# Performance work log

Measured on AMD Instinct MI355X. Metric: run time of the kernel, lower is better.

Reference implementation:

```python
import jax, jax.numpy as jnp
import numpy as np

HIDDEN = 2048
NUM_HEADS = 16
HEAD_DIM = HIDDEN // NUM_HEADS


def setup_inputs() -> dict:
    key = jax.random.key(0)
    ks = jax.random.split(key, 5)
    B, S, H = 2, 2048, HIDDEN
    # xavier_uniform bounds
    qkv_bound = float(np.sqrt(6.0 / (H + 3 * H)))
    out_bound = float(np.sqrt(6.0 / (H + H)))
    return {
        "x": jax.random.normal(ks[0], (B, S, H), dtype=jnp.float32),
        "W_qkv": jax.random.uniform(ks[1], (3 * H, H), minval=-qkv_bound, maxval=qkv_bound, dtype=jnp.float32),
        "b_qkv": jnp.zeros((3 * H,), dtype=jnp.float32),
        "W_out": jax.random.uniform(ks[2], (H, H), minval=-out_bound, maxval=out_bound, dtype=jnp.float32),
        "b_out": jnp.zeros((H,), dtype=jnp.float32),
    }


def reference(x, W_qkv, b_qkv, W_out, b_out):
    B, S, H = x.shape
    # fused QKV projection (torch Linear: x @ W.T + b)
    qkv = x @ W_qkv.T + b_qkv                      # (B, S, 3H)
    q, k, v = jnp.split(qkv, 3, axis=-1)
    # (B, S, H) -> (B, N, S, D)
    def to_heads(t):
        return t.reshape(B, S, NUM_HEADS, HEAD_DIM).transpose(0, 2, 1, 3)
    q, k, v = to_heads(q), to_heads(k), to_heads(v)
    scale = HEAD_DIM ** -0.5
    scores = jnp.einsum("bnqd,bnkd->bnqk", q, k) * scale  # (B, N, S, S)
    causal = jnp.triu(jnp.ones((S, S), dtype=bool), k=1)
    scores = jnp.where(causal, -jnp.inf, scores)
    attn = jax.nn.softmax(scores, axis=-1)
    out = jnp.einsum("bnqk,bnkd->bnqd", attn, v)           # (B, N, S, D)
    out = out.transpose(0, 2, 1, 3).reshape(B, S, H)
    return out @ W_out.T + b_out
```

## Files before the change

### kernel.cpp

```cpp
#include <hip/hip_runtime.h>
#include <stdint.h>


using bf16x8 = __attribute__((ext_vector_type(8))) __bf16;
using f32x4  = __attribute__((ext_vector_type(4))) float;

#define S_LEN 2048
#define HID   2048
#define NHEAD 16
#define DHEAD 128
#define KDIM  2048
#define QSCALE_L2E (0.08838834764831845f * 1.4426950408889634f)

__device__ __forceinline__ unsigned short f2bf(float f) {
  union { float f; unsigned int u; } c; c.f = f;
  unsigned int u = c.u;
  return (unsigned short)((u + 0x7FFFu + ((u >> 16) & 1u)) >> 16);
}

__device__ __forceinline__ unsigned int pkbf(float a, float b) {
  union { __bf16 h[2]; unsigned int u; } x;
  x.h[0] = (__bf16)a; x.h[1] = (__bf16)b;
  return x.u;
}

__device__ __forceinline__ void gload_lds16(const void* g, void* l) {
  __builtin_amdgcn_global_load_lds(
      (const __attribute__((address_space(1))) unsigned int*)g,
      (__attribute__((address_space(3))) unsigned int*)l, 16, 0, 0);
}

__device__ __forceinline__ f32x4 mfma16(bf16x8 a, bf16x8 b, f32x4 c) {
  return __builtin_amdgcn_mfma_f32_16x16x32_bf16(a, b, c, 0, 0, 0);
}

__device__ __forceinline__ float hmax4(f32x4 v) {
  return fmaxf(fmaxf(v[0], v[1]), fmaxf(v[2], v[3]));
}

__global__ void cvt_bf16(const float* __restrict__ in, unsigned short* __restrict__ out, int n) {
  const int n4 = n >> 2;
  const int stride = gridDim.x * blockDim.x;
  for (int i = blockIdx.x * blockDim.x + threadIdx.x; i < n4; i += stride) {
    float4 v = reinterpret_cast<const float4*>(in)[i];
    ushort4 o;
    o.x = f2bf(v.x); o.y = f2bf(v.y); o.z = f2bf(v.z); o.w = f2bf(v.w);
    reinterpret_cast<ushort4*>(out)[i] = o;
  }
}

__global__ __launch_bounds__(512, 2) void gemm_qkv8(
    const unsigned short* __restrict__ A, const unsigned short* __restrict__ Bw,
    const float* __restrict__ bias,
    unsigned short* __restrict__ q_out, unsigned short* __restrict__ k_out,
    unsigned short* __restrict__ vt_out)
{
  __shared__ char lsA[2][32768];
  __shared__ char lsB[2][32768];
  const int tid = threadIdx.x, l = tid & 63, w = tid >> 6;
  const int wr = w >> 2, wc = w & 3;
  const int row16 = l & 15, kg = l >> 4;

  const int bid = blockIdx.x;
  const int swz = (bid & 7) * 48 + (bid >> 3);
  const int bm = (swz & 15) * 256, bn = (swz >> 4) * 256;
  const char* Ag = (const char*)A + (size_t)bm * (KDIM * 2);
  const char* Bg = (const char*)Bw + (size_t)bn * (KDIM * 2);

  f32x4 acc[8][4] = {};

  float bv[4];
  #pragma unroll
  for (int j = 0; j < 4; ++j) bv[j] = bias[bn + wc * 64 + j * 16 + row16];
  asm volatile("" :: "v"(bv[0]), "v"(bv[1]), "v"(bv[2]), "v"(bv[3]));

#define BAR   asm volatile("s_barrier" ::: "memory")
#define LGKM0 asm volatile("s_waitcnt lgkmcnt(0)" ::: "memory"); __builtin_amdgcn_sched_barrier(0)
#define VM4   asm volatile("s_waitcnt vmcnt(4)" ::: "memory")
#define PRIO1 __builtin_amdgcn_s_setprio(1)
#define PRIO0 __builtin_amdgcn_s_setprio(0)

#define STAGE_A(buf, k0, qa) do {                                              \
    _Pragma("unroll")                                                          \
    for (int p = 0; p < 2; ++p) {                                              \
      const int o = tid * 16;                                                  \
      const int r = p * 128 + (qa) * 64 + (o >> 7);                            \
      const int cb = (o & 127) ^ ((r & 7) << 4);                               \
      gload_lds16(Ag + (size_t)r * (KDIM * 2) + (k0) * 2 + cb,                 \
                  lsA[buf] + p * 16384 + (qa) * 8192 + o);                     \
    } } while (0)

#define STAGE_B(buf, k0, qb) do {                                              \
    _Pragma("unroll")                                                          \
    for (int p = 0; p < 2; ++p) {                                              \
      const int o = tid * 16;                                                  \
      const int blk = o >> 12;                                                 \
      const int r = p * 128 + blk * 64 + (qb) * 32 + ((o >> 7) & 31);          \
      const int cb = (o & 127) ^ ((r & 7) << 4);                               \
      gload_lds16(Bg + (size_t)r * (KDIM * 2) + (k0) * 2 + cb,                 \
                  lsB[buf] + p * 16384 + blk * 8192 + (qb) * 4096 + (o & 4095)); \
    } } while (0)

#define RD_A(dst, i0) do { _Pragma("unroll")                                   \
    for (int i = 0; i < 4; ++i) {                                              \
      const int m = wr * 128 + ((i0) + i) * 16 + row16;                        \
      _Pragma("unroll")                                                        \
      for (int h = 0; h < 2; ++h)                                              \
        dst[i][h] = *(const bf16x8*)(Ac + m * 128 + ((h * 64 + kg * 16) ^ ((m & 7) << 4))); \
    } } while (0)

#define RD_B(dst, j0) do { _Pragma("unroll")                                   \
    for (int j = 0; j < 2; ++j) {                                              \
      const int n = wc * 64 + ((j0) + j) * 16 + row16;                         \
      _Pragma("unroll")                                                        \
      for (int h = 0; h < 2; ++h)                                              \
        dst[j][h] = *(const bf16x8*)(Bc + n * 128 + ((h * 64 + kg * 16) ^ ((n & 7) << 4))); \
    } } while (0)

#define MM(afrag, bfrag, i0, j0) do { _Pragma("unroll")                        \
    for (int i = 0; i < 4; ++i) { _Pragma("unroll")                            \
      for (int j = 0; j < 2; ++j) { _Pragma("unroll")                          \
        for (int h = 0; h < 2; ++h)                                            \
          acc[(i0) + i][(j0) + j] = mfma16(afrag[i][h], bfrag[j][h], acc[(i0) + i][(j0) + j]); \
    } } } while (0)

  STAGE_A(0, 0, 0); STAGE_B(0, 0, 0); STAGE_A(0, 0, 1); STAGE_B(0, 0, 1);
  asm volatile("s_waitcnt vmcnt(0)" ::: "memory");
  BAR;

  bf16x8 afl[4][2], afh[4][2], bfl[2][2], bfh[2][2];
  constexpr int NCH = KDIM / 64;

  #pragma unroll 1
  for (int t = 0; t < NCH - 1; ++t) {
    const int cur = t & 1, nxt = cur ^ 1;
    const char* Ac = lsA[cur];
    const char* Bc = lsB[cur];
    const int k1 = (t + 1) * 64;
    RD_A(afl, 0); RD_B(bfl, 0);
    STAGE_A(nxt, k1, 0);
    BAR; LGKM0;
    PRIO1; MM(afl, bfl, 0, 0); PRIO0;
    VM4; BAR;
    RD_A(afh, 4);
    STAGE_B(nxt, k1, 0);
    BAR; LGKM0;
    PRIO1; MM(afh, bfl, 4, 0); PRIO0;
    VM4; BAR;
    RD_B(bfh, 2);
    STAGE_A(nxt, k1, 1);
    BAR; LGKM0;
    PRIO1; MM(afl, bfh, 0, 2); PRIO0;
    BAR;
    STAGE_B(nxt, k1, 1);
    BAR;
    PRIO1; MM(afh, bfh, 4, 2); PRIO0;
    VM4; BAR;
  }
  {
    const char* Ac = lsA[(NCH - 1) & 1];
    const char* Bc = lsB[(NCH - 1) & 1];
    RD_A(afl, 0); RD_B(bfl, 0);
    MM(afl, bfl, 0, 0);
    asm volatile("s_waitcnt vmcnt(2)" ::: "memory");
    RD_A(afh, 4);
    MM(afh, bfl, 4, 0);
    asm volatile("s_waitcnt vmcnt(0)" ::: "memory");
    RD_B(bfh, 2);
    MM(afl, bfh, 0, 2);
    MM(afh, bfh, 4, 2);
  }
#undef STAGE_A
#undef STAGE_B
#undef RD_A
#undef RD_B
#undef MM
#undef BAR
#undef LGKM0
#undef VM4
#undef PRIO1
#undef PRIO0

  #pragma unroll
  for (int i = 0; i < 8; ++i) {
    const int row = bm + wr * 128 + i * 16 + kg * 4;
    #pragma unroll
    for (int j = 0; j < 4; ++j) {
      const int col = bn + wc * 64 + j * 16 + row16;
      const int sec = col >> 11;
      const int within = col & 2047;
      const int head = within >> 7, d = within & 127;
      #pragma unroll
      for (int r = 0; r < 4; ++r) {
        const int rr = row + r;
        const int b = rr >> 11, s = rr & 2047;
        const int bh = b * NHEAD + head;
        const float v = acc[i][j][r] + bv[j];
        if (sec == 0)
          q_out[((size_t)bh * S_LEN + s) * DHEAD + d] = f2bf(v * QSCALE_L2E);
        else if (sec == 1)
          k_out[((size_t)bh * S_LEN + s) * DHEAD + d] = f2bf(v);
        else
          vt_out[((size_t)bh * DHEAD + d) * S_LEN + s] = f2bf(v);
      }
    }
  }
}

__global__ __launch_bounds__(256) void gemm_out(
    const unsigned short* __restrict__ A, const unsigned short* __restrict__ Bw,
    const float* __restrict__ bias, float* __restrict__ c_out)
{
  constexpr int K = KDIM, N = HID;
  __shared__ char lsA[128 * 128];
  __shared__ char lsB[128 * 128];
  const int tid = threadIdx.x;
  const int l = tid & 63, w = tid >> 6;
  const int wr = w >> 1, wc = w & 1;
  const int bm = blockIdx.x * 128, bn = blockIdx.y * 128;
  const int row16 = l & 15, kg = l >> 4;

  f32x4 acc[4][4] = {};

  for (int k0 = 0; k0 < K; k0 += 64) {
    #pragma unroll
    for (int c = 0; c < 4; ++c) {
      const int o = c * 4096 + tid * 16;
      const int r = o >> 7;
      const int cb = (o & 127) ^ ((r & 7) << 4);
      gload_lds16((const char*)A + ((size_t)(bm + r) * K + k0) * 2 + cb,
                  lsA + c * 4096 + (w << 10));
      gload_lds16((const char*)Bw + ((size_t)(bn + r) * K + k0) * 2 + cb,
                  lsB + c * 4096 + (w << 10));
    }
    __syncthreads();

    #pragma unroll
    for (int h = 0; h < 2; ++h) {
      bf16x8 af[4], bfr[4];
      #pragma unroll
      for (int i = 0; i < 4; ++i) {
        const int ra = wr * 64 + i * 16 + row16;
        af[i]  = *(const bf16x8*)(lsA + ra * 128 + ((h * 64 + kg * 16) ^ ((ra & 7) << 4)));
        const int rb = wc * 64 + i * 16 + row16;
        bfr[i] = *(const bf16x8*)(lsB + rb * 128 + ((h * 64 + kg * 16) ^ ((rb & 7) << 4)));
      }
      #pragma unroll
      for (int i = 0; i < 4; ++i)
        #pragma unroll
        for (int j = 0; j < 4; ++j)
          acc[i][j] = mfma16(af[i], bfr[j], acc[i][j]);
    }
    __syncthreads();
  }

  #pragma unroll
  for (int i = 0; i < 4; ++i) {
    const int row = bm + wr * 64 + i * 16 + kg * 4;
    #pragma unroll
    for (int j = 0; j < 4; ++j) {
      const int col = bn + wc * 64 + j * 16 + row16;
      const float bvj = bias[col];
      #pragma unroll
      for (int r = 0; r < 4; ++r)
        c_out[(size_t)(row + r) * N + col] = acc[i][j][r] + bvj;
    }
  }
}

__global__ __launch_bounds__(256, 2) void attn_fwd(
    const unsigned short* __restrict__ Q, const unsigned short* __restrict__ Kk,
    const unsigned short* __restrict__ Vt, unsigned short* __restrict__ O)
{
  __shared__ char lsK[2][64 * 256];
  __shared__ char lsV[2][128 * 128];
  __shared__ char lsP[4][32 * 128];
  const int tid = threadIdx.x, l = tid & 63, w = tid >> 6;
  const int row16 = l & 15, kg = l >> 4;
  const int qb = (blockIdx.y < 16) ? (15 - (int)blockIdx.x) : (int)blockIdx.x;
  const int bh = blockIdx.y;
  const int bidx = bh >> 4, head = bh & 15;

  const char* Qh = (const char*)(Q  + (size_t)bh * S_LEN * DHEAD);
  const char* Kh = (const char*)(Kk + (size_t)bh * S_LEN * DHEAD);
  const char* Vh = (const char*)(Vt + (size_t)bh * DHEAD * S_LEN);

  const int q0w = qb * 128 + w * 32;

  bf16x8 qf[2][4];
  #pragma unroll
  for (int qs = 0; qs < 2; ++qs)
    #pragma unroll
    for (int t = 0; t < 4; ++t)
      qf[qs][t] = *(const bf16x8*)(Qh + ((size_t)(q0w + qs * 16 + row16) * DHEAD + t * 32 + kg * 8) * 2);

  float m[2]  = {-1e30f, -1e30f};
  float ls[2] = {0.f, 0.f};
  f32x4 oacc[2][8] = {};

  const int last = 2 * qb + 1;

#define STAGE(buf, kt_) do {                                                     \
    _Pragma("unroll")                                                            \
    for (int c = 0; c < 4; ++c) {                                                \
      const int o = c * 4096 + tid * 16;                                         \
      const int rk = o >> 8, cbk = (o & 255) ^ ((rk & 7) << 4);                  \
      gload_lds16(Kh + (size_t)((kt_) * 64 + rk) * 256 + cbk,                    \
                  lsK[buf] + c * 4096 + (w << 10));                              \
      const int dv = o >> 7, cbv = (o & 127) ^ ((dv & 7) << 4);                  \
      gload_lds16(Vh + (size_t)dv * 4096 + (size_t)(kt_) * 128 + cbv,            \
                  lsV[buf] + c * 4096 + (w << 10));                              \
    } } while (0)

  STAGE(0, 0);
  __syncthreads();

  int cur = 0;
  for (int kt = 0; ; ++kt) {
    if (kt < last) STAGE(cur ^ 1, kt + 1);

    if (kt * 64 <= q0w + 31) {
      const char* Kc = lsK[cur];
      const char* Vc = lsV[cur];
      char* Pl = lsP[w];

      f32x4 sc[4][2] = {};
      #pragma unroll
      for (int j = 0; j < 4; ++j) {
        const int krow = j * 16 + row16;
        const int sw = (krow & 7) << 4;
        bf16x8 kf[4];
        #pragma unroll
        for (int t = 0; t < 4; ++t)
          kf[t] = *(const bf16x8*)(Kc + krow * 256 + ((t * 64 + kg * 16) ^ sw));
        #pragma unroll
        for (int t = 0; t < 4; ++t) {
          sc[j][0] = mfma16(kf[t], qf[0][t], sc[j][0]);
          sc[j][1] = mfma16(kf[t], qf[1][t], sc[j][1]);
        }
      }

      if (kt >= 2 * qb) {
        #pragma unroll
        for (int j = 0; j < 4; ++j) {
          const int kvb = kt * 64 + j * 16 + kg * 4;
          #pragma unroll
          for (int qs = 0; qs < 2; ++qs) {
            const int qq = q0w + qs * 16 + row16;
            #pragma unroll
            for (int r = 0; r < 4; ++r)
              if (kvb + r > qq) sc[j][qs][r] = -1e30f;
          }
        }
      }

      float pm[2], al[2] = {1.f, 1.f};
      #pragma unroll
      for (int qs = 0; qs < 2; ++qs) {
        float mx = fmaxf(fmaxf(hmax4(sc[0][qs]), hmax4(sc[1][qs])),
                         fmaxf(hmax4(sc[2][qs]), hmax4(sc[3][qs])));
        mx = fmaxf(mx, __shfl_xor(mx, 16, 64));
        mx = fmaxf(mx, __shfl_xor(mx, 32, 64));
        pm[qs] = mx;
      }
      const bool need = (pm[0] > m[0] + 8.f) || (pm[1] > m[1] + 8.f);
      if (__any(need)) {
        const float n0 = fmaxf(m[0], pm[0]), n1 = fmaxf(m[1], pm[1]);
        al[0] = exp2f(m[0] - n0); al[1] = exp2f(m[1] - n1);
        m[0] = n0; m[1] = n1;
        float aq[2][4];
        #pragma unroll
        for (int qs2 = 0; qs2 < 2; ++qs2)
          #pragma unroll
          for (int r = 0; r < 4; ++r)
            aq[qs2][r] = __shfl(al[qs2], kg * 4 + r, 64);
        #pragma unroll
        for (int qs2 = 0; qs2 < 2; ++qs2)
          #pragma unroll
          for (int dt = 0; dt < 8; ++dt)
            #pragma unroll
            for (int r = 0; r < 4; ++r)
              oacc[qs2][dt][r] *= aq[qs2][r];
      }

      #pragma unroll
      for (int qs = 0; qs < 2; ++qs) {
        const int q = qs * 16 + row16;
        const int psw = (q & 7) << 4;
        float ps = 0.f;
        #pragma unroll
        for (int j = 0; j < 4; ++j) {
          const float p0 = exp2f(sc[j][qs][0] - m[qs]);
          const float p1 = exp2f(sc[j][qs][1] - m[qs]);
          const float p2 = exp2f(sc[j][qs][2] - m[qs]);
          const float p3 = exp2f(sc[j][qs][3] - m[qs]);
          ps += (p0 + p1) + (p2 + p3);
          uint2 pw; pw.x = pkbf(p0, p1); pw.y = pkbf(p2, p3);
          *(uint2*)(Pl + q * 128 + ((j * 32 + kg * 8) ^ psw)) = pw;
        }
        ps += __shfl_xor(ps, 16, 64);
        ps += __shfl_xor(ps, 32, 64);
        ls[qs] = ls[qs] * al[qs] + ps;
      }

      bf16x8 pa[2][2];
      #pragma unroll
      for (int qs2 = 0; qs2 < 2; ++qs2) {
        const int q = qs2 * 16 + row16;
        #pragma unroll
        for (int ks = 0; ks < 2; ++ks)
          pa[qs2][ks] = *(const bf16x8*)(Pl + q * 128 + ((ks * 64 + kg * 16) ^ ((q & 7) << 4)));
      }
      #pragma unroll
      for (int dt = 0; dt < 8; ++dt) {
        const int drow = dt * 16 + row16;
        const int vsw = (drow & 7) << 4;
        bf16x8 v0 = *(const bf16x8*)(Vc + drow * 128 + ((kg * 16) ^ vsw));
        bf16x8 v1 = *(const bf16x8*)(Vc + drow * 128 + ((64 + kg * 16) ^ vsw));
        oacc[0][dt] = mfma16(pa[0][0], v0, oacc[0][dt]);
        oacc[0][dt] = mfma16(pa[0][1], v1, oacc[0][dt]);
        oacc[1][dt] = mfma16(pa[1][0], v0, oacc[1][dt]);
        oacc[1][dt] = mfma16(pa[1][1], v1, oacc[1][dt]);
      }
    }

    __syncthreads();
    if (kt == last) break;
    cur ^= 1;
  }
#undef STAGE

  #pragma unroll
  for (int qs2 = 0; qs2 < 2; ++qs2) {
    #pragma unroll
    for (int r = 0; r < 4; ++r) {
      const float lr = __shfl(ls[qs2], kg * 4 + r, 64);
      const float inv = 1.0f / lr;
      const int q = q0w + qs2 * 16 + kg * 4 + r;
      const size_t orow = (size_t)(bidx * S_LEN + q) * HID + (size_t)head * DHEAD;
      #pragma unroll
      for (int dt = 0; dt < 8; ++dt)
        O[orow + dt * 16 + row16] = f2bf(oacc[qs2][dt][r] * inv);
    }
  }
}

extern "C" void kernel_launch(void* const* d_in, const int* in_sizes, int n_in,
                              void* d_out, int out_size, void* d_ws, size_t ws_size,
                              hipStream_t stream) {
  const float* x    = (const float*)d_in[0];
  const float* Wqkv = (const float*)d_in[1];
  const float* bqkv = (const float*)d_in[2];
  const float* Wout = (const float*)d_in[3];
  const float* bout = (const float*)d_in[4];
  float* out = (float*)d_out;

  if (ws_size < 100663296) return;
  char* ws = (char*)d_ws;
  unsigned short* Qb    = (unsigned short*)(ws);
  unsigned short* Kb    = (unsigned short*)(ws + 16777216);
  unsigned short* Vtb   = (unsigned short*)(ws + 2 * 16777216);
  unsigned short* xb    = (unsigned short*)(ws + 3 * 16777216);
  unsigned short* Ob    = xb;
  unsigned short* Wqkvb = (unsigned short*)(ws + 4 * 16777216);
  unsigned short* Woutb = (unsigned short*)(ws + 4 * 16777216 + 25165824);

  cvt_bf16<<<2048, 256, 0, stream>>>(x,    xb,    4096 * 2048);
  cvt_bf16<<<2048, 256, 0, stream>>>(Wqkv, Wqkvb, 6144 * 2048);
  cvt_bf16<<<1024, 256, 0, stream>>>(Wout, Woutb, 2048 * 2048);

  gemm_qkv8<<<384, 512, 0, stream>>>(xb, Wqkvb, bqkv, Qb, Kb, Vtb);
  attn_fwd<<<dim3(16, 32), 256, 0, stream>>>(Qb, Kb, Vtb, Ob);
  gemm_out<<<dim3(32, 16), 256, 0, stream>>>(Ob, Woutb, bout, out);
}
```

Before: 317.4 us.

## Deepen QKV GEMM prefetch pipeline with half-tile LDS staging and unrolled loop

Restructures the QKV projection GEMM's shared-memory staging so each buffer is split into independently loaded halves. Prefetch now runs up to one and a half chunks ahead instead of one, with vmcnt(6) waits. The main loop is unrolled by two so buffer indices are compile-time constants, and the bias load moves into the epilogue. The goal is to hide global-load latency behind MFMA work, at the cost of more complex barrier ordering and more in-flight loads that could race if the waits are miscounted.

Measured after the change: 314.0 us. No clear change (-1.1%).

```diff
diff --git a/kernel.cpp b/kernel.cpp
--- a/kernel.cpp
+++ b/kernel.cpp
@@ -49,7 +49,14 @@
   }
 }
 
-__global__ __launch_bounds__(512, 2) void gemm_qkv8(
+#define BAR   asm volatile("s_barrier" ::: "memory")
+#define LGKM0 do { asm volatile("s_waitcnt lgkmcnt(0)" ::: "memory"); \
+                   __builtin_amdgcn_sched_barrier(0); } while (0)
+#define VM(n) asm volatile("s_waitcnt vmcnt(" #n ")" ::: "memory")
+#define PRIO1 __builtin_amdgcn_s_setprio(1)
+#define PRIO0 __builtin_amdgcn_s_setprio(0)
+
+__global__ __launch_bounds__(512, 2) void gemm_qkv(
     const unsigned short* __restrict__ A, const unsigned short* __restrict__ Bw,
     const float* __restrict__ bias,
     unsigned short* __restrict__ q_out, unsigned short* __restrict__ k_out,
@@ -69,139 +76,166 @@
 
   f32x4 acc[8][4] = {};
 
-  float bv[4];
-  #pragma unroll
-  for (int j = 0; j < 4; ++j) bv[j] = bias[bn + wc * 64 + j * 16 + row16];
-  asm volatile("" :: "v"(bv[0]), "v"(bv[1]), "v"(bv[2]), "v"(bv[3]));
-
-#define BAR   asm volatile("s_barrier" ::: "memory")
-#define LGKM0 asm volatile("s_waitcnt lgkmcnt(0)" ::: "memory"); __builtin_amdgcn_sched_barrier(0)
-#define VM4   asm volatile("s_waitcnt vmcnt(4)" ::: "memory")
-#define PRIO1 __builtin_amdgcn_s_setprio(1)
-#define PRIO0 __builtin_amdgcn_s_setprio(0)
-
-#define STAGE_A(buf, k0, qa) do {                                              \
-    _Pragma("unroll")                                                          \
+#define STAGE_A(cc, h) do { _Pragma("unroll")                                  \
     for (int p = 0; p < 2; ++p) {                                              \
-      const int o = tid * 16;                                                  \
-      const int r = p * 128 + (qa) * 64 + (o >> 7);                            \
-      const int cb = (o & 127) ^ ((r & 7) << 4);                               \
-      gload_lds16(Ag + (size_t)r * (KDIM * 2) + (k0) * 2 + cb,                 \
-                  lsA[buf] + p * 16384 + (qa) * 8192 + o);                     \
+      const int o = p * 8192 + tid * 16;                                       \
+      const int lr = o >> 7;                                                   \
+      const int m = ((lr >> 6) << 7) + (h) * 64 + (lr & 63);                   \
+      const int cb = (o & 127) ^ ((m & 7) << 4);                               \
+      gload_lds16(Ag + (size_t)m * (KDIM * 2) + (size_t)(cc) * 128 + cb,       \
+                  lsA[(cc) & 1] + (h) * 16384 + p * 8192 + (w << 10));         \
     } } while (0)
 
-#define STAGE_B(buf, k0, qb) do {                                              \
-    _Pragma("unroll")                                                          \
+#define STAGE_B(cc, h) do { _Pragma("unroll")                                  \
     for (int p = 0; p < 2; ++p) {                                              \
-      const int o = tid * 16;                                                  \
-      const int blk = o >> 12;                                                 \
-      const int r = p * 128 + blk * 64 + (qb) * 32 + ((o >> 7) & 31);          \
-      const int cb = (o & 127) ^ ((r & 7) << 4);                               \
-      gload_lds16(Bg + (size_t)r * (KDIM * 2) + (k0) * 2 + cb,                 \
-                  lsB[buf] + p * 16384 + blk * 8192 + (qb) * 4096 + (o & 4095)); \
+      const int o = p * 8192 + tid * 16;                                       \
+      const int lr = o >> 7;                                                   \
+      const int n = ((lr >> 5) << 6) + (h) * 32 + (lr & 31);                   \
+      const int cb = (o & 127) ^ ((n & 7) << 4);                               \
+      gload_lds16(Bg + (size_t)n * (KDIM * 2) + (size_t)(cc) * 128 + cb,       \
+                  lsB[(cc) & 1] + (h) * 16384 + p * 8192 + (w << 10));         \
     } } while (0)
 
-#define RD_A(dst, i0) do { _Pragma("unroll")                                   \
+#define RD_A(dst, i0, buf) do { _Pragma("unroll")                              \
     for (int i = 0; i < 4; ++i) {                                              \
       const int m = wr * 128 + ((i0) + i) * 16 + row16;                        \
+      const char* base = lsA[buf] + (((m >> 6) & 1) * 16384)                   \
+                       + (((m >> 7) & 1) * 8192) + ((m & 63) * 128);           \
       _Pragma("unroll")                                                        \
       for (int h = 0; h < 2; ++h)                                              \
-        dst[i][h] = *(const bf16x8*)(Ac + m * 128 + ((h * 64 + kg * 16) ^ ((m & 7) << 4))); \
+        dst[i][h] = *(const bf16x8*)(base +                                    \
+                    ((h * 64 + kg * 16) ^ ((m & 7) << 4)));                    \
     } } while (0)
 
-#define RD_B(dst, j0) do { _Pragma("unroll")                                   \
+#define RD_B(dst, j0, buf) do { _Pragma("unroll")                              \
     for (int j = 0; j < 2; ++j) {                                              \
       const int n = wc * 64 + ((j0) + j) * 16 + row16;                         \
+      const char* base = lsB[buf] + (((n >> 5) & 1) * 16384)                   \
+                       + ((n >> 6) * 4096) + ((n & 31) * 128);                 \
       _Pragma("unroll")                                                        \
       for (int h = 0; h < 2; ++h)                                              \
-        dst[j][h] = *(const bf16x8*)(Bc + n * 128 + ((h * 64 + kg * 16) ^ ((n & 7) << 4))); \
+        dst[j][h] = *(const bf16x8*)(base +                                    \
+                    ((h * 64 + kg * 16) ^ ((n & 7) << 4)));                    \
     } } while (0)
 
-#define MM(afrag, bfrag, i0, j0) do { _Pragma("unroll")                        \
+#define MM(af, bf, i0, j0) do { _Pragma("unroll")                              \
     for (int i = 0; i < 4; ++i) { _Pragma("unroll")                            \
       for (int j = 0; j < 2; ++j) { _Pragma("unroll")                          \
         for (int h = 0; h < 2; ++h)                                            \
-          acc[(i0) + i][(j0) + j] = mfma16(afrag[i][h], bfrag[j][h], acc[(i0) + i][(j0) + j]); \
+          acc[(i0) + i][(j0) + j] =                                            \
+            mfma16(af[i][h], bf[j][h], acc[(i0) + i][(j0) + j]);               \
     } } } while (0)
 
-  STAGE_A(0, 0, 0); STAGE_B(0, 0, 0); STAGE_A(0, 0, 1); STAGE_B(0, 0, 1);
-  asm volatile("s_waitcnt vmcnt(0)" ::: "memory");
+  STAGE_A(0, 0); STAGE_B(0, 0); STAGE_A(0, 1); STAGE_B(0, 1);
+  STAGE_A(1, 0); STAGE_B(1, 0); STAGE_A(1, 1);
+  VM(6);
   BAR;
 
-  bf16x8 afl[4][2], afh[4][2], bfl[2][2], bfh[2][2];
-  constexpr int NCH = KDIM / 64;
+  bf16x8 alo[4][2], ahi[4][2], blo[2][2], bhi[2][2];
 
   #pragma unroll 1
-  for (int t = 0; t < NCH - 1; ++t) {
-    const int cur = t & 1, nxt = cur ^ 1;
-    const char* Ac = lsA[cur];
-    const char* Bc = lsB[cur];
-    const int k1 = (t + 1) * 64;
-    RD_A(afl, 0); RD_B(bfl, 0);
-    STAGE_A(nxt, k1, 0);
-    BAR; LGKM0;
-    PRIO1; MM(afl, bfl, 0, 0); PRIO0;
-    VM4; BAR;
-    RD_A(afh, 4);
-    STAGE_B(nxt, k1, 0);
-    BAR; LGKM0;
-    PRIO1; MM(afh, bfl, 4, 0); PRIO0;
-    VM4; BAR;
-    RD_B(bfh, 2);
-    STAGE_A(nxt, k1, 1);
-    BAR; LGKM0;
-    PRIO1; MM(afl, bfh, 0, 2); PRIO0;
-    BAR;
-    STAGE_B(nxt, k1, 1);
-    BAR;
-    PRIO1; MM(afh, bfh, 4, 2); PRIO0;
-    VM4; BAR;
+  for (int i = 0; i < 15; ++i) {
+    const int t0 = 2 * i;
+    RD_A(alo, 0, 0); RD_B(blo, 0, 0);
+    STAGE_B(t0 + 1, 1);
+    BAR; LGKM0;
+    PRIO1; MM(alo, blo, 0, 0); PRIO0;
+    BAR;
+    RD_A(ahi, 4, 0);
+    STAGE_A(t0 + 2, 0);
+    BAR; LGKM0;
+    PRIO1; MM(ahi, blo, 4, 0); PRIO0;
+    BAR;
+    RD_B(bhi, 2, 0);
+    STAGE_B(t0 + 2, 0);
+    BAR; LGKM0;
+    PRIO1; MM(alo, bhi, 0, 2); PRIO0;
+    BAR;
+    STAGE_A(t0 + 2, 1);
+    BAR;
+    PRIO1; MM(ahi, bhi, 4, 2); PRIO0;
+    VM(6);
+    BAR;
+    RD_A(alo, 0, 1); RD_B(blo, 0, 1);
+    STAGE_B(t0 + 2, 1);
+    BAR; LGKM0;
+    PRIO1; MM(alo, blo, 0, 0); PRIO0;
+    BAR;
+    RD_A(ahi, 4, 1);
+    STAGE_A(t0 + 3, 0);
+    BAR; LGKM0;
+    PRIO1; MM(ahi, blo, 4, 0); PRIO0;
+    BAR;
+    RD_B(bhi, 2, 1);
+    STAGE_B(t0 + 3, 0);
+    BAR; LGKM0;
+    PRIO1; MM(alo, bhi, 0, 2); PRIO0;
+    BAR;
+    STAGE_A(t0 + 3, 1);
+    BAR;
+    PRIO1; MM(ahi, bhi, 4, 2); PRIO0;
+    VM(6);
+    BAR;
   }
   {
-    const char* Ac = lsA[(NCH - 1) & 1];
-    const char* Bc = lsB[(NCH - 1) & 1];
-    RD_A(afl, 0); RD_B(bfl, 0);
-    MM(afl, bfl, 0, 0);
-    asm volatile("s_waitcnt vmcnt(2)" ::: "memory");
-    RD_A(afh, 4);
-    MM(afh, bfl, 4, 0);
-    asm volatile("s_waitcnt vmcnt(0)" ::: "memory");
-    RD_B(bfh, 2);
-    MM(afl, bfh, 0, 2);
-    MM(afh, bfh, 4, 2);
+    RD_A(alo, 0, 0); RD_B(blo, 0, 0);
+    STAGE_B(31, 1);
+    BAR; LGKM0;
+    PRIO1; MM(alo, blo, 0, 0); PRIO0;
+    BAR;
+    RD_A(ahi, 4, 0);
+    BAR; LGKM0;
+    PRIO1; MM(ahi, blo, 4, 0); PRIO0;
+    BAR;
+    RD_B(bhi, 2, 0);
+    BAR; LGKM0;
+    PRIO1; MM(alo, bhi, 0, 2); PRIO0;
+    BAR;
+    PRIO1; MM(ahi, bhi, 4, 2); PRIO0;
+    VM(2);
+    BAR;
+    RD_A(alo, 0, 1); RD_B(blo, 0, 1);
+    BAR; LGKM0;
+    PRIO1; MM(alo, blo, 0, 0); PRIO0;
+    BAR;
+    RD_A(ahi, 4, 1);
+    BAR; LGKM0;
+    PRIO1; MM(ahi, blo, 4, 0); PRIO0;
+    VM(0);
+    BAR;
+    RD_B(bhi, 2, 1);
+    LGKM0;
+    PRIO1; MM(alo, bhi, 0, 2); PRIO0;
+    PRIO1; MM(ahi, bhi, 4, 2); PRIO0;
   }
 #undef STAGE_A
 #undef STAGE_B
 #undef RD_A
 #undef RD_B
 #undef MM
-#undef BAR
-#undef LGKM0
-#undef VM4
-#undef PRIO1
-#undef PRIO0
 
   #pragma unroll
-  for (int i = 0; i < 8; ++i) {
-    const int row = bm + wr * 128 + i * 16 + kg * 4;
+  for (int j = 0; j < 4; ++j) {
+    const int col = bn + wc * 64 + j * 16 + row16;
+    const float bvj = bias[col];
+    const int sec = col >> 11;
+    const int within = col & 2047;
+    const int head = within >> 7, d = within & 127;
     #pragma unroll
-    for (int j = 0; j < 4; ++j) {
-      const int col = bn + wc * 64 + j * 16 + row16;
-      const int sec = col >> 11;
-      const int within = col & 2047;
-      const int head = within >> 7, d = within & 127;
+    for (int i = 0; i < 8; ++i) {
+      const int row = bm + wr * 128 + i * 16 + kg * 4;
       #pragma unroll
       for (int r = 0; r < 4; ++r) {
         const int rr = row + r;
         const int b = rr >> 11, s = rr & 2047;
-        const int bh = b * NHEAD + head;
-        const float v = acc[i][j][r] + bv[j];
+        const int bh2 = b * NHEAD + head;
+        const float v = acc[i][j][r] + bvj;
         if (sec == 0)
-          q_out[((size_t)bh * S_LEN + s) * DHEAD + d] = f2bf(v * QSCALE_L2E);
+          q_out[((size_t)bh2 * S_LEN + s) * DHEAD + d] = f2bf(v * QSCALE_L2E);
         else if (sec == 1)
-          k_out[((size_t)bh * S_LEN + s) * DHEAD + d] = f2bf(v);
+          k_out[((size_t)bh2 * S_LEN + s) * DHEAD + d] = f2bf(v);
         else
-          vt_out[((size_t)bh * DHEAD + d) * S_LEN + s] = f2bf(v);
+          vt_out[((size_t)bh2 * DHEAD + d) * S_LEN + s] = f2bf(v);
       }
     }
   }
@@ -469,7 +503,7 @@
   cvt_bf16<<<2048, 256, 0, stream>>>(Wqkv, Wqkvb, 6144 * 2048);
   cvt_bf16<<<1024, 256, 0, stream>>>(Wout, Woutb, 2048 * 2048);
 
-  gemm_qkv8<<<384, 512, 0, stream>>>(xb, Wqkvb, bqkv, Qb, Kb, Vtb);
+  gemm_qkv<<<384, 512, 0, stream>>>(xb, Wqkvb, bqkv, Qb, Kb, Vtb);
   attn_fwd<<<dim3(16, 32), 256, 0, stream>>>(Qb, Kb, Vtb, Ob);
   gemm_out<<<dim3(32, 16), 256, 0, stream>>>(Ob, Woutb, bout, out);
 }
```
